# Performance work log

Hardware: AMD Instinct MI355X
Metric: run time of the kernel (lower is better)

The kernel has to match this reference:

```python
import jax, jax.numpy as jnp
import numpy as np

N, D, B, H = 131072, 512, 512, 8  # nodes, hidden_dim, graphs, heads


def setup_inputs() -> dict:
    key = jax.random.key(0)
    ks = jax.random.split(key, 4)
    x = jax.random.normal(ks[0], (N, D), jnp.float32)
    # sorted segment ids; every graph nonempty (matches torch batch.max()+1 semantics)
    batch = jnp.sort(jnp.arange(N, dtype=jnp.int32) % B)
    query = jax.random.normal(ks[1], (D,), jnp.float32)          # nn.Parameter(randn(1,1,D))
    W_in = jax.random.normal(ks[2], (3 * D, D), jnp.float32) / np.sqrt(D)  # MHA in_proj_weight
    b_in = jnp.zeros((3 * D,), jnp.float32)
    W_out = jax.random.normal(ks[3], (D, D), jnp.float32) / np.sqrt(D)     # MHA out_proj
    b_out = jnp.zeros((D,), jnp.float32)
    return {"x": x, "batch": batch, "num_graphs": B, "query": query,
            "W_in": W_in, "b_in": b_in, "W_out": W_out, "b_out": b_out}


def reference(x, batch, num_graphs, query, W_in, b_in, W_out, b_out):
    # Fused ragged single-query multihead attention pooling (eval mode: dropout off).
    D = x.shape[1]
    dh = D // H
    scale = 1.0 / np.sqrt(dh)
    # q/k/v projections (torch MHA packed in_proj: rows [0:D]=q, [D:2D]=k, [2D:3D]=v)
    q = ((query @ W_in[:D].T + b_in[:D]) * scale).reshape(H, dh)       # [H, dh], shared across graphs
    k = (x @ W_in[D:2 * D].T + b_in[D:2 * D]).reshape(-1, H, dh)       # [N, H, dh]
    v = (x @ W_in[2 * D:].T + b_in[2 * D:]).reshape(-1, H, dh)         # [N, H, dh]
    scores = jnp.einsum('nhd,hd->nh', k, q)                             # [N, H]
    # segment (per-graph) softmax over nodes
    smax = jax.ops.segment_max(scores, batch, num_segments=num_graphs)  # [B, H]
    e = jnp.exp(scores - smax[batch])
    denom = jax.ops.segment_sum(e, batch, num_segments=num_graphs)      # [B, H]
    p = e / denom[batch]                                                # [N, H]
    pooled = jax.ops.segment_sum(p[:, :, None] * v, batch, num_segments=num_graphs)  # [B, H, dh]
    return pooled.reshape(num_graphs, D) @ W_out.T + b_out              # [B, D]
```

## Files before the change

### kernel.cpp

```cpp
#include <hip/hip_runtime.h>
#include <math.h>

#define NHEAD 8

typedef __fp16 half2v __attribute__((ext_vector_type(2)));

template <int CTRL>
__device__ __forceinline__ float dpp_add(float v) {
    int r = __builtin_amdgcn_mov_dpp(__float_as_int(v), CTRL, 0xF, 0xF, false);
    return v + __int_as_float(r);
}

__device__ __forceinline__ float swap16_add(float v) {
    int a = __float_as_int(v);
    int b;
    asm volatile("v_mov_b32 %1, %0\n\t"
                 "s_nop 1\n\t"
                 "v_permlane16_swap_b32 %0, %1\n\t"
                 "s_nop 1"
                 : "+v"(a), "=&v"(b));
    return __int_as_float(a) + __int_as_float(b);
}
__device__ __forceinline__ float swap32_add(float v) {
    int a = __float_as_int(v);
    int b;
    asm volatile("v_mov_b32 %1, %0\n\t"
                 "s_nop 1\n\t"
                 "v_permlane32_swap_b32 %0, %1\n\t"
                 "s_nop 1"
                 : "+v"(a), "=&v"(b));
    return __int_as_float(a) + __int_as_float(b);
}

__device__ __forceinline__ float wave_allsum(float v) {
    v = dpp_add<0xB1>(v);
    v = dpp_add<0x4E>(v);
    v = dpp_add<0x141>(v);
    v = dpp_add<0x140>(v);
    v = swap16_add(v);
    v = swap32_add(v);
    return v;
}

__global__ void __launch_bounds__(256) k_setup(const float* __restrict__ query,
                                               const float* __restrict__ W_in,
                                               const float* __restrict__ b_in,
                                               const int* __restrict__ batch,
                                               float* __restrict__ wsc,
                                               int* __restrict__ seg_start,
                                               int* __restrict__ seg_end,
                                               int N, float scale) {
    const int g = blockIdx.x, t = threadIdx.x;
    if (g < 16) {
        __shared__ float qs4[64][4];
        __shared__ float qs[64];
        const int h = g >> 1, half = g & 1;
        {
            const int d = t & 63, qtr = t >> 6;
            const int row = h * 64 + d;
            const float4* wq = reinterpret_cast<const float4*>(W_in + (size_t)row * 512 + qtr * 128);
            const float4* qv = reinterpret_cast<const float4*>(query + qtr * 128);
            float a = 0.f;
#pragma unroll 8
            for (int i = 0; i < 32; ++i) {
                float4 w = wq[i], q = qv[i];
                a += w.x * q.x + w.y * q.y + w.z * q.z + w.w * q.w;
            }
            qs4[d][qtr] = a;
        }
        __syncthreads();
        if (t < 64) {
            const float s = qs4[t][0] + qs4[t][1] + qs4[t][2] + qs4[t][3];
            qs[t] = (s + b_in[h * 64 + t]) * scale;
        }
        __syncthreads();
        const int i = half * 256 + t;
        const float* Wk = W_in + (size_t)512 * 512;
        float a = 0.f;
#pragma unroll 8
        for (int d = 0; d < 64; ++d)
            a += qs[d] * Wk[(size_t)(h * 64 + d) * 512 + i];
        wsc[h * 512 + i] = a;
    } else {
        const int stride = (gridDim.x - 16) * 256;
        for (int n = (g - 16) * 256 + t; n < N; n += stride) {
            int b = batch[n];
            if (n == 0 || batch[n - 1] != b) seg_start[b] = n;
            if (n == N - 1 || batch[n + 1] != b) seg_end[b] = n + 1;
        }
    }
}

__global__ void __launch_bounds__(256, 3) k_fused1(const float* __restrict__ x,
                                                   const float* __restrict__ wsc,
                                                   const int* __restrict__ seg_start,
                                                   const int* __restrict__ seg_end,
                                                   float* __restrict__ xp_part,
                                                   float* __restrict__ denom_part,
                                                   int nc) {
    __shared__ float mrg[4][32][64];
    __shared__ float dsum[4][NHEAD];
    const int b = blockIdx.x, c = blockIdx.y, t = threadIdx.x;
    const int lane = t & 63, w = t >> 6;
    const int s0 = seg_start[b], s1 = seg_end[b];
    const int len = s1 - s0;
    const int clen = (len + nc - 1) / nc;
    const int c0r = s0 + c * clen;
    const int c1r = min(s1, c0r + clen);
    const int wlen = (c1r - c0r + 3) >> 2;
    const int r0 = c0r + w * wlen;
    const int r1 = min(c1r, r0 + wlen);

    half2v wh[NHEAD][4];
#pragma unroll
    for (int h = 0; h < NHEAD; ++h) {
        const float4 wa = *reinterpret_cast<const float4*>(wsc + h * 512 + lane * 8);
        const float4 wb = *reinterpret_cast<const float4*>(wsc + h * 512 + lane * 8 + 4);
        wh[h][0] = __builtin_amdgcn_cvt_pkrtz(wa.x, wa.y);
        wh[h][1] = __builtin_amdgcn_cvt_pkrtz(wa.z, wa.w);
        wh[h][2] = __builtin_amdgcn_cvt_pkrtz(wb.x, wb.y);
        wh[h][3] = __builtin_amdgcn_cvt_pkrtz(wb.z, wb.w);
    }

    float acc[NHEAD][8];
#pragma unroll
    for (int h = 0; h < NHEAD; ++h)
#pragma unroll
        for (int j = 0; j < 8; ++j) acc[h][j] = 0.f;
    float dacc[NHEAD];
#pragma unroll
    for (int h = 0; h < NHEAD; ++h) dacc[h] = 0.f;

    const float* xl = x + lane * 8;
#define LD0(r) (*reinterpret_cast<const float4*>(xl + (size_t)(r) * 512))
#define LD1(r) (*reinterpret_cast<const float4*>(xl + (size_t)(r) * 512 + 4))

    float4 a0, a1, n0, n1;
    if (r0 + 0 < r1) { a0 = LD0(r0 + 0); a1 = LD1(r0 + 0); }
    if (r0 + 1 < r1) { n0 = LD0(r0 + 1); n1 = LD1(r0 + 1); }

    for (int r = r0; r < r1; ++r) {
        const float4 c0 = a0, c1 = a1;
        a0 = n0; a1 = n1;
        if (r + 2 < r1) { n0 = LD0(r + 2); n1 = LD1(r + 2); }

        const half2v xh0 = __builtin_amdgcn_cvt_pkrtz(c0.x, c0.y);
        const half2v xh1 = __builtin_amdgcn_cvt_pkrtz(c0.z, c0.w);
        const half2v xh2 = __builtin_amdgcn_cvt_pkrtz(c1.x, c1.y);
        const half2v xh3 = __builtin_amdgcn_cvt_pkrtz(c1.z, c1.w);

        float e[NHEAD];
#pragma unroll
        for (int h = 0; h < NHEAD; ++h) {
            float d = __builtin_amdgcn_fdot2(xh0, wh[h][0], 0.f, false);
            d = __builtin_amdgcn_fdot2(xh1, wh[h][1], d, false);
            d = __builtin_amdgcn_fdot2(xh2, wh[h][2], d, false);
            d = __builtin_amdgcn_fdot2(xh3, wh[h][3], d, false);
            e[h] = __expf(wave_allsum(d));
        }
#pragma unroll
        for (int h = 0; h < NHEAD; ++h) {
            dacc[h] += e[h];
            acc[h][0] += e[h] * c0.x; acc[h][1] += e[h] * c0.y;
            acc[h][2] += e[h] * c0.z; acc[h][3] += e[h] * c0.w;
            acc[h][4] += e[h] * c1.x; acc[h][5] += e[h] * c1.y;
            acc[h][6] += e[h] * c1.z; acc[h][7] += e[h] * c1.w;
        }
    }
#undef LD0
#undef LD1

    float* pb = xp_part + (size_t)(b * nc + c) * (NHEAD * 512);
    if (lane == 0) {
#pragma unroll
        for (int h = 0; h < NHEAD; ++h) dsum[w][h] = dacc[h];
    }
#pragma unroll
    for (int h = 0; h < 4; ++h)
#pragma unroll
        for (int j = 0; j < 8; ++j)
            mrg[w][h * 8 + j][lane] = acc[h][j];
    __syncthreads();
    {
        const int c0i = 2 * t;
        const int lsrc = c0i >> 3, slot = c0i & 7;
#pragma unroll
        for (int h = 0; h < 4; ++h) {
            float num0 = 0.f, num1 = 0.f;
#pragma unroll
            for (int g = 0; g < 4; ++g) {
                num0 += mrg[g][h * 8 + slot][lsrc];
                num1 += mrg[g][h * 8 + slot + 1][lsrc];
            }
            float2 o = {num0, num1};
            *reinterpret_cast<float2*>(pb + (size_t)h * 512 + c0i) = o;
        }
    }
    __syncthreads();
#pragma unroll
    for (int h = 4; h < NHEAD; ++h)
#pragma unroll
        for (int j = 0; j < 8; ++j)
            mrg[w][(h - 4) * 8 + j][lane] = acc[h][j];
    __syncthreads();
    {
        const int c0i = 2 * t;
        const int lsrc = c0i >> 3, slot = c0i & 7;
#pragma unroll
        for (int h = 4; h < NHEAD; ++h) {
            float num0 = 0.f, num1 = 0.f;
#pragma unroll
            for (int g = 0; g < 4; ++g) {
                num0 += mrg[g][(h - 4) * 8 + slot][lsrc];
                num1 += mrg[g][(h - 4) * 8 + slot + 1][lsrc];
            }
            float2 o = {num0, num1};
            *reinterpret_cast<float2*>(pb + (size_t)h * 512 + c0i) = o;
        }
    }
    if (t < NHEAD)
        denom_part[(b * nc + c) * NHEAD + t] = dsum[0][t] + dsum[1][t] + dsum[2][t] + dsum[3][t];
}

__global__ void __launch_bounds__(256) k_merge(const float* __restrict__ xp_part,
                                               const float* __restrict__ denom_part,
                                               float* __restrict__ xp, int nc) {
    const int b = blockIdx.x, t = threadIdx.x;
    __shared__ float rd[NHEAD];
    if (t < NHEAD) {
        float d = 0.f;
        for (int c = 0; c < nc; ++c) d += denom_part[(b * nc + c) * NHEAD + t];
        rd[t] = 1.f / d;
    }
    __syncthreads();
    const float2* src = reinterpret_cast<const float2*>(xp_part + (size_t)b * nc * NHEAD * 512);
    float2* dst = reinterpret_cast<float2*>(xp + (size_t)b * NHEAD * 512);
#pragma unroll
    for (int i = 0; i < 8; ++i) {
        const int idx = i * 256 + t;
        const int h = idx >> 8;
        float2 s = src[idx];
        for (int c = 1; c < nc; ++c) {
            const float2 v = src[(size_t)c * NHEAD * 256 + idx];
            s.x += v.x; s.y += v.y;
        }
        const float r = rd[h];
        s.x *= r; s.y *= r;
        dst[idx] = s;
    }
}

__global__ void __launch_bounds__(256) k_gemm_tn4w(const float* __restrict__ A, int lda, int zA,
                                                   const float* __restrict__ Bm, int ldb, int zB,
                                                   const float* __restrict__ bias, int zBias,
                                                   float* __restrict__ C, int ldc, int zC, int K) {
    __shared__ float As[4][32][36];
    __shared__ float Bs[4][32][36];
    __shared__ float red[4][32][32];
    const int z = blockIdx.z;
    A += (size_t)z * zA;
    Bm += (size_t)z * zB;
    bias += (size_t)z * zBias;
    C += (size_t)z * zC;
    const int m0 = blockIdx.x * 32, n0 = blockIdx.y * 32;
    const int t = threadIdx.x;
    const int w = t >> 6, lane = t & 63;
    const int row = lane >> 1, c0 = (lane & 1) * 16;
    const int ty = lane >> 3, tx = lane & 7;
    const int Kw = K >> 2;
    const int kw0 = w * Kw;
    float c[4][4];
#pragma unroll
    for (int i = 0; i < 4; ++i)
#pragma unroll
        for (int j = 0; j < 4; ++j) c[i][j] = 0.f;

    for (int kt = 0; kt < Kw; kt += 32) {
        const int k0 = kw0 + kt;
        const float* Ar = A + (size_t)(m0 + row) * lda + k0 + c0;
        const float* Br = Bm + (size_t)(n0 + row) * ldb + k0 + c0;
        float4 a4[4], b4[4];
#pragma unroll
        for (int j = 0; j < 4; ++j) {
            a4[j] = *reinterpret_cast<const float4*>(Ar + j * 4);
            b4[j] = *reinterpret_cast<const float4*>(Br + j * 4);
        }
#pragma unroll
        for (int j = 0; j < 4; ++j) {
            As[w][c0 + j * 4 + 0][row] = a4[j].x;
            As[w][c0 + j * 4 + 1][row] = a4[j].y;
            As[w][c0 + j * 4 + 2][row] = a4[j].z;
            As[w][c0 + j * 4 + 3][row] = a4[j].w;
            Bs[w][c0 + j * 4 + 0][row] = b4[j].x;
            Bs[w][c0 + j * 4 + 1][row] = b4[j].y;
            Bs[w][c0 + j * 4 + 2][row] = b4[j].z;
            Bs[w][c0 + j * 4 + 3][row] = b4[j].w;
        }
#pragma unroll
        for (int kk = 0; kk < 32; ++kk) {
            float4 av = *reinterpret_cast<const float4*>(&As[w][kk][ty * 4]);
            float4 bv = *reinterpret_cast<const float4*>(&Bs[w][kk][tx * 4]);
            c[0][0] += av.x * bv.x; c[0][1] += av.x * bv.y; c[0][2] += av.x * bv.z; c[0][3] += av.x * bv.w;
            c[1][0] += av.y * bv.x; c[1][1] += av.y * bv.y; c[1][2] += av.y * bv.z; c[1][3] += av.y * bv.w;
            c[2][0] += av.z * bv.x; c[2][1] += av.z * bv.y; c[2][2] += av.z * bv.z; c[2][3] += av.z * bv.w;
            c[3][0] += av.w * bv.x; c[3][1] += av.w * bv.y; c[3][2] += av.w * bv.z; c[3][3] += av.w * bv.w;
        }
    }
#pragma unroll
    for (int i = 0; i < 4; ++i)
#pragma unroll
        for (int j = 0; j < 4; ++j) red[w][ty * 4 + i][tx * 4 + j] = c[i][j];
    __syncthreads();
    const int r = t >> 3, cc = (t & 7) * 4;
    float4 s = {0.f, 0.f, 0.f, 0.f};
#pragma unroll
    for (int g = 0; g < 4; ++g) {
        const float4 v = *reinterpret_cast<const float4*>(&red[g][r][cc]);
        s.x += v.x; s.y += v.y; s.z += v.z; s.w += v.w;
    }
    const float4 bv4 = *reinterpret_cast<const float4*>(bias + n0 + cc);
    float4 o = {s.x + bv4.x, s.y + bv4.y, s.z + bv4.z, s.w + bv4.w};
    *reinterpret_cast<float4*>(C + (size_t)(m0 + r) * ldc + n0 + cc) = o;
}

extern "C" void kernel_launch(void* const* d_in, const int* in_sizes, int n_in,
                              void* d_out, int out_size, void* d_ws, size_t ws_size,
                              hipStream_t stream) {
    const float* x     = (const float*)d_in[0];
    const int*   batch = (const int*)d_in[1];
    const float* query = (const float*)d_in[3];
    const float* W_in  = (const float*)d_in[4];
    const float* b_in  = (const float*)d_in[5];
    const float* W_out = (const float*)d_in[6];
    const float* b_out = (const float*)d_in[7];
    float* out = (float*)d_out;

    const int D = in_sizes[3];
    const int N = in_sizes[0] / D;
    const int B = out_size / D;
    const int dh = D / NHEAD;
    const float scale = 1.0f / sqrtf((float)dh);

    float* wsf       = (float*)d_ws;
    float* wsc       = wsf;
    float* xp        = wsc + NHEAD * 512;
    float* pooled    = xp + (size_t)B * NHEAD * 512;
    float* denom_ws  = pooled + (size_t)B * 512;
    int*   seg_start = (int*)(denom_ws + (size_t)B * 4 * NHEAD);
    int*   seg_end   = seg_start + B;
    float* tail      = (float*)(seg_end + B);

    const size_t usedFloats = (size_t)(tail - wsf);
    const size_t avail = ws_size / 4 - usedFloats;
    int nc = 1;
    float* xp_part = xp;
    if (avail >= (size_t)B * 3 * NHEAD * 512) {
        nc = 3;
        xp_part = tail;
    }

    k_setup<<<16 + 256, 256, 0, stream>>>(query, W_in, b_in, batch, wsc,
                                          seg_start, seg_end, N, scale);

    k_fused1<<<dim3(B, nc), 256, 0, stream>>>(x, wsc, seg_start, seg_end,
                                              xp_part, denom_ws, nc);

    k_merge<<<B, 256, 0, stream>>>(xp_part, denom_ws, xp, nc);

    k_gemm_tn4w<<<dim3(B / 32, dh / 32, NHEAD), 256, 0, stream>>>(
        xp, NHEAD * 512, 512,
        W_in + (size_t)2 * D * D, D, dh * D,
        b_in + 2 * D, dh,
        pooled, D, dh, D);

    k_gemm_tn4w<<<dim3(B / 32, D / 32, 1), 256, 0, stream>>>(
        pooled, D, 0,
        W_out, D, 0,
        b_out, 0,
        out, D, 0, D);
}
```

Measured before the change: 110.2 us.

## Fuse split-chunk merge and normalization into the V-projection GEMM

Drops the separate merge kernel: the per-head V-projection GEMM now sums the chunk partials and applies the reciprocal softmax denominator while loading its A tile. The chunk count drops from three to two and the fused pooling kernel's launch bound rises to four blocks per SM, with the per-head exp consumed straight into the accumulators inside one loop. The aim is to save one launch and the round trip of the merged buffer. The GEMM now re-reads the partials once per N tile, and a dead, half-finished kernel (k_fused2) is left in the file.

```diff
diff --git a/kernel.cpp b/kernel.cpp
--- a/kernel.cpp
+++ b/kernel.cpp
@@ -91,7 +91,7 @@
     }
 }
 
-__global__ void __launch_bounds__(256, 3) k_fused1(const float* __restrict__ x,
+__global__ void __launch_bounds__(256, 4) k_fused2(const float* __restrict__ x,
                                                    const float* __restrict__ wsc,
                                                    const int* __restrict__ seg_start,
                                                    const int* __restrict__ seg_end,
@@ -127,9 +127,7 @@
     for (int h = 0; h < NHEAD; ++h)
 #pragma unroll
         for (int j = 0; j < 8; ++j) acc[h][j] = 0.f;
-    float dacc[NHEAD];
-#pragma unroll
-    for (int h = 0; h < NHEAD; ++h) dacc[h] = 0.f;
+    float dacc = 0.f;
 
     const float* xl = x + lane * 8;
 #define LD0(r) (*reinterpret_cast<const float4*>(xl + (size_t)(r) * 512))
@@ -149,22 +147,18 @@
         const half2v xh2 = __builtin_amdgcn_cvt_pkrtz(c1.x, c1.y);
         const half2v xh3 = __builtin_amdgcn_cvt_pkrtz(c1.z, c1.w);
 
-        float e[NHEAD];
 #pragma unroll
         for (int h = 0; h < NHEAD; ++h) {
             float d = __builtin_amdgcn_fdot2(xh0, wh[h][0], 0.f, false);
             d = __builtin_amdgcn_fdot2(xh1, wh[h][1], d, false);
             d = __builtin_amdgcn_fdot2(xh2, wh[h][2], d, false);
             d = __builtin_amdgcn_fdot2(xh3, wh[h][3], d, false);
-            e[h] = __expf(wave_allsum(d));
-        }
-#pragma unroll
-        for (int h = 0; h < NHEAD; ++h) {
-            dacc[h] += e[h];
-            acc[h][0] += e[h] * c0.x; acc[h][1] += e[h] * c0.y;
-            acc[h][2] += e[h] * c0.z; acc[h][3] += e[h] * c0.w;
-            acc[h][4] += e[h] * c1.x; acc[h][5] += e[h] * c1.y;
-            acc[h][6] += e[h] * c1.z; acc[h][7] += e[h] * c1.w;
+            const float e = __expf(wave_allsum(d));
+            dacc += e;
+            acc[h][0] += e * c0.x; acc[h][1] += e * c0.y;
+            acc[h][2] += e * c0.z; acc[h][3] += e * c0.w;
+            acc[h][4] += e * c1.x; acc[h][5] += e * c1.y;
+            acc[h][6] += e * c1.z; acc[h][7] += e * c1.w;
         }
     }
 #undef LD0
@@ -172,8 +166,90 @@
 
     float* pb = xp_part + (size_t)(b * nc + c) * (NHEAD * 512);
     if (lane == 0) {
-#pragma unroll
-        for (int h = 0; h < NHEAD; ++h) dsum[w][h] = dacc[h];
+    }
+    (void)pb;
+
+}
+
+__global__ void __launch_bounds__(256, 4) k_fused2b(const float* __restrict__ x,
+                                                    const float* __restrict__ wsc,
+                                                    const int* __restrict__ seg_start,
+                                                    const int* __restrict__ seg_end,
+                                                    float* __restrict__ xp_part,
+                                                    float* __restrict__ denom_part,
+                                                    int nc) {
+    __shared__ float mrg[4][32][64];
+    __shared__ float dsum[4][NHEAD];
+    const int b = blockIdx.x, c = blockIdx.y, t = threadIdx.x;
+    const int lane = t & 63, w = t >> 6;
+    const int s0 = seg_start[b], s1 = seg_end[b];
+    const int len = s1 - s0;
+    const int clen = (len + nc - 1) / nc;
+    const int c0r = s0 + c * clen;
+    const int c1r = min(s1, c0r + clen);
+    const int wlen = (c1r - c0r + 3) >> 2;
+    const int r0 = c0r + w * wlen;
+    const int r1 = min(c1r, r0 + wlen);
+
+    half2v wh[NHEAD][4];
+#pragma unroll
+    for (int h = 0; h < NHEAD; ++h) {
+        const float4 wa = *reinterpret_cast<const float4*>(wsc + h * 512 + lane * 8);
+        const float4 wb = *reinterpret_cast<const float4*>(wsc + h * 512 + lane * 8 + 4);
+        wh[h][0] = __builtin_amdgcn_cvt_pkrtz(wa.x, wa.y);
+        wh[h][1] = __builtin_amdgcn_cvt_pkrtz(wa.z, wa.w);
+        wh[h][2] = __builtin_amdgcn_cvt_pkrtz(wb.x, wb.y);
+        wh[h][3] = __builtin_amdgcn_cvt_pkrtz(wb.z, wb.w);
+    }
+
+    float acc[NHEAD][8];
+#pragma unroll
+    for (int h = 0; h < NHEAD; ++h)
+#pragma unroll
+        for (int j = 0; j < 8; ++j) acc[h][j] = 0.f;
+    float dh[NHEAD];
+#pragma unroll
+    for (int h = 0; h < NHEAD; ++h) dh[h] = 0.f;
+
+    const float* xl = x + lane * 8;
+#define LD0(r) (*reinterpret_cast<const float4*>(xl + (size_t)(r) * 512))
+#define LD1(r) (*reinterpret_cast<const float4*>(xl + (size_t)(r) * 512 + 4))
+
+    float4 a0, a1, n0, n1;
+    if (r0 + 0 < r1) { a0 = LD0(r0 + 0); a1 = LD1(r0 + 0); }
+    if (r0 + 1 < r1) { n0 = LD0(r0 + 1); n1 = LD1(r0 + 1); }
+
+    for (int r = r0; r < r1; ++r) {
+        const float4 c0 = a0, c1 = a1;
+        a0 = n0; a1 = n1;
+        if (r + 2 < r1) { n0 = LD0(r + 2); n1 = LD1(r + 2); }
+
+        const half2v xh0 = __builtin_amdgcn_cvt_pkrtz(c0.x, c0.y);
+        const half2v xh1 = __builtin_amdgcn_cvt_pkrtz(c0.z, c0.w);
+        const half2v xh2 = __builtin_amdgcn_cvt_pkrtz(c1.x, c1.y);
+        const half2v xh3 = __builtin_amdgcn_cvt_pkrtz(c1.z, c1.w);
+
+#pragma unroll
+        for (int h = 0; h < NHEAD; ++h) {
+            float d = __builtin_amdgcn_fdot2(xh0, wh[h][0], 0.f, false);
+            d = __builtin_amdgcn_fdot2(xh1, wh[h][1], d, false);
+            d = __builtin_amdgcn_fdot2(xh2, wh[h][2], d, false);
+            d = __builtin_amdgcn_fdot2(xh3, wh[h][3], d, false);
+            const float e = __expf(wave_allsum(d));
+            dh[h] += e;
+            acc[h][0] += e * c0.x; acc[h][1] += e * c0.y;
+            acc[h][2] += e * c0.z; acc[h][3] += e * c0.w;
+            acc[h][4] += e * c1.x; acc[h][5] += e * c1.y;
+            acc[h][6] += e * c1.z; acc[h][7] += e * c1.w;
+        }
+    }
+#undef LD0
+#undef LD1
+
+    float* pb = xp_part + (size_t)(b * nc + c) * (NHEAD * 512);
+    if (lane == 0) {
+#pragma unroll
+        for (int h = 0; h < NHEAD; ++h) dsum[w][h] = dh[h];
     }
 #pragma unroll
     for (int h = 0; h < 4; ++h)
@@ -222,46 +298,103 @@
         denom_part[(b * nc + c) * NHEAD + t] = dsum[0][t] + dsum[1][t] + dsum[2][t] + dsum[3][t];
 }
 
-__global__ void __launch_bounds__(256) k_merge(const float* __restrict__ xp_part,
-                                               const float* __restrict__ denom_part,
-                                               float* __restrict__ xp, int nc) {
-    const int b = blockIdx.x, t = threadIdx.x;
-    __shared__ float rd[NHEAD];
-    if (t < NHEAD) {
-        float d = 0.f;
-        for (int c = 0; c < nc; ++c) d += denom_part[(b * nc + c) * NHEAD + t];
-        rd[t] = 1.f / d;
-    }
-    __syncthreads();
-    const float2* src = reinterpret_cast<const float2*>(xp_part + (size_t)b * nc * NHEAD * 512);
-    float2* dst = reinterpret_cast<float2*>(xp + (size_t)b * NHEAD * 512);
-#pragma unroll
-    for (int i = 0; i < 8; ++i) {
-        const int idx = i * 256 + t;
-        const int h = idx >> 8;
-        float2 s = src[idx];
-        for (int c = 1; c < nc; ++c) {
-            const float2 v = src[(size_t)c * NHEAD * 256 + idx];
-            s.x += v.x; s.y += v.y;
-        }
-        const float r = rd[h];
-        s.x *= r; s.y *= r;
-        dst[idx] = s;
-    }
-}
-
-__global__ void __launch_bounds__(256) k_gemm_tn4w(const float* __restrict__ A, int lda, int zA,
-                                                   const float* __restrict__ Bm, int ldb, int zB,
-                                                   const float* __restrict__ bias, int zBias,
-                                                   float* __restrict__ C, int ldc, int zC, int K) {
+__global__ void __launch_bounds__(256) k_gemm_xp(const float* __restrict__ xp_part,
+                                                 const float* __restrict__ denom_part,
+                                                 const float* __restrict__ Bm,
+                                                 const float* __restrict__ bias,
+                                                 float* __restrict__ C,
+                                                 int nc) {
     __shared__ float As[4][32][36];
     __shared__ float Bs[4][32][36];
     __shared__ float red[4][32][32];
+    __shared__ float rdv[32];
     const int z = blockIdx.z;
-    A += (size_t)z * zA;
-    Bm += (size_t)z * zB;
-    bias += (size_t)z * zBias;
-    C += (size_t)z * zC;
+    const int m0 = blockIdx.x * 32, n0 = blockIdx.y * 32;
+    const int t = threadIdx.x;
+    const int w = t >> 6, lane = t & 63;
+    const int row = lane >> 1, c0 = (lane & 1) * 16;
+    const int ty = lane >> 3, tx = lane & 7;
+    const int Kw = 128;
+    const int kw0 = w * Kw;
+
+    const float* Bz = Bm + (size_t)z * 64 * 512;
+    const float* biasz = bias + z * 64;
+    float* Cz = C + z * 64;
+
+    if (t < 32) {
+        float d = 0.f;
+        for (int c = 0; c < nc; ++c)
+            d += denom_part[((m0 + t) * nc + c) * NHEAD + z];
+        rdv[t] = 1.f / d;
+    }
+    __syncthreads();
+
+    float cc[4][4];
+#pragma unroll
+    for (int i = 0; i < 4; ++i)
+#pragma unroll
+        for (int j = 0; j < 4; ++j) cc[i][j] = 0.f;
+
+    for (int kt = 0; kt < Kw; kt += 32) {
+        const int k0 = kw0 + kt;
+        const float rl = rdv[row];
+        float4 a4[4], b4[4];
+#pragma unroll
+        for (int j = 0; j < 4; ++j) {
+            float4 s = {0.f, 0.f, 0.f, 0.f};
+            for (int c = 0; c < nc; ++c) {
+                const float4 v = *reinterpret_cast<const float4*>(
+                    xp_part + (size_t)(((m0 + row) * nc + c) * NHEAD + z) * 512 + k0 + c0 + j * 4);
+                s.x += v.x; s.y += v.y; s.z += v.z; s.w += v.w;
+            }
+            a4[j].x = s.x * rl; a4[j].y = s.y * rl; a4[j].z = s.z * rl; a4[j].w = s.w * rl;
+            b4[j] = *reinterpret_cast<const float4*>(Bz + (size_t)(n0 + row) * 512 + k0 + c0 + j * 4);
+        }
+#pragma unroll
+        for (int j = 0; j < 4; ++j) {
+            As[w][c0 + j * 4 + 0][row] = a4[j].x;
+            As[w][c0 + j * 4 + 1][row] = a4[j].y;
+            As[w][c0 + j * 4 + 2][row] = a4[j].z;
+            As[w][c0 + j * 4 + 3][row] = a4[j].w;
+            Bs[w][c0 + j * 4 + 0][row] = b4[j].x;
+            Bs[w][c0 + j * 4 + 1][row] = b4[j].y;
+            Bs[w][c0 + j * 4 + 2][row] = b4[j].z;
+            Bs[w][c0 + j * 4 + 3][row] = b4[j].w;
+        }
+#pragma unroll
+        for (int kk = 0; kk < 32; ++kk) {
+            float4 av = *reinterpret_cast<const float4*>(&As[w][kk][ty * 4]);
+            float4 bv = *reinterpret_cast<const float4*>(&Bs[w][kk][tx * 4]);
+            cc[0][0] += av.x * bv.x; cc[0][1] += av.x * bv.y; cc[0][2] += av.x * bv.z; cc[0][3] += av.x * bv.w;
+            cc[1][0] += av.y * bv.x; cc[1][1] += av.y * bv.y; cc[1][2] += av.y * bv.z; cc[1][3] += av.y * bv.w;
+            cc[2][0] += av.z * bv.x; cc[2][1] += av.z * bv.y; cc[2][2] += av.z * bv.z; cc[2][3] += av.z * bv.w;
+            cc[3][0] += av.w * bv.x; cc[3][1] += av.w * bv.y; cc[3][2] += av.w * bv.z; cc[3][3] += av.w * bv.w;
+        }
+    }
+#pragma unroll
+    for (int i = 0; i < 4; ++i)
+#pragma unroll
+        for (int j = 0; j < 4; ++j) red[w][ty * 4 + i][tx * 4 + j] = cc[i][j];
+    __syncthreads();
+    const int r = t >> 3, ccx = (t & 7) * 4;
+    float4 s = {0.f, 0.f, 0.f, 0.f};
+#pragma unroll
+    for (int g = 0; g < 4; ++g) {
+        const float4 v = *reinterpret_cast<const float4*>(&red[g][r][ccx]);
+        s.x += v.x; s.y += v.y; s.z += v.z; s.w += v.w;
+    }
+    const float4 bv4 = *reinterpret_cast<const float4*>(biasz + n0 + ccx);
+    float4 o = {s.x + bv4.x, s.y + bv4.y, s.z + bv4.z, s.w + bv4.w};
+    *reinterpret_cast<float4*>(Cz + (size_t)(m0 + r) * 512 + n0 + ccx) = o;
+}
+
+__global__ void __launch_bounds__(256) k_gemm_tn4w(const float* __restrict__ A, int lda,
+                                                   const float* __restrict__ Bm, int ldb,
+                                                   const float* __restrict__ bias,
+                                                   float* __restrict__ C, int ldc, int K) {
+    __shared__ float As[4][32][36];
+    __shared__ float Bs[4][32][36];
+    __shared__ float red[4][32][32];
     const int m0 = blockIdx.x * 32, n0 = blockIdx.y * 32;
     const int t = threadIdx.x;
     const int w = t >> 6, lane = t & 63;
@@ -338,44 +471,34 @@
     const int D = in_sizes[3];
     const int N = in_sizes[0] / D;
     const int B = out_size / D;
-    const int dh = D / NHEAD;
-    const float scale = 1.0f / sqrtf((float)dh);
+    const float scale = 1.0f / sqrtf(64.0f);
 
     float* wsf       = (float*)d_ws;
     float* wsc       = wsf;
-    float* xp        = wsc + NHEAD * 512;
-    float* pooled    = xp + (size_t)B * NHEAD * 512;
+    float* pooled    = wsc + NHEAD * 512;
     float* denom_ws  = pooled + (size_t)B * 512;
-    int*   seg_start = (int*)(denom_ws + (size_t)B * 4 * NHEAD);
+    int*   seg_start = (int*)(denom_ws + (size_t)B * 2 * NHEAD);
     int*   seg_end   = seg_start + B;
-    float* tail      = (float*)(seg_end + B);
-
-    const size_t usedFloats = (size_t)(tail - wsf);
+    float* xp_part   = (float*)(seg_end + B);
+
+    const size_t usedFloats = (size_t)(xp_part - wsf);
     const size_t avail = ws_size / 4 - usedFloats;
-    int nc = 1;
-    float* xp_part = xp;
-    if (avail >= (size_t)B * 3 * NHEAD * 512) {
-        nc = 3;
-        xp_part = tail;
-    }
+    const int nc = (avail >= (size_t)B * 2 * NHEAD * 512) ? 2 : 1;
 
     k_setup<<<16 + 256, 256, 0, stream>>>(query, W_in, b_in, batch, wsc,
                                           seg_start, seg_end, N, scale);
 
-    k_fused1<<<dim3(B, nc), 256, 0, stream>>>(x, wsc, seg_start, seg_end,
-                                              xp_part, denom_ws, nc);
-
-    k_merge<<<B, 256, 0, stream>>>(xp_part, denom_ws, xp, nc);
-
-    k_gemm_tn4w<<<dim3(B / 32, dh / 32, NHEAD), 256, 0, stream>>>(
-        xp, NHEAD * 512, 512,
-        W_in + (size_t)2 * D * D, D, dh * D,
-        b_in + 2 * D, dh,
-        pooled, D, dh, D);
+    k_fused2b<<<dim3(B, nc), 256, 0, stream>>>(x, wsc, seg_start, seg_end,
+                                               xp_part, denom_ws, nc);
+
+    k_gemm_xp<<<dim3(B / 32, 2, NHEAD), 256, 0, stream>>>(
+        xp_part, denom_ws,
+        W_in + (size_t)2 * D * D, b_in + 2 * D,
+        pooled, nc);
 
     k_gemm_tn4w<<<dim3(B / 32, D / 32, 1), 256, 0, stream>>>(
-        pooled, D, 0,
-        W_out, D, 0,
-        b_out, 0,
-        out, D, 0, D);
-}
+        pooled, D,
+        W_out, D,
+        b_out,
+        out, D, D);
+}
```

Result: slower. 184.8 us (+67.7%).
